# Kernel tuning notes

Measured on AMD Instinct MI355X. Metric: run time of the kernel, lower is better.

The kernel has to match this reference:

```python
import jax, jax.numpy as jnp
import numpy as np

N = 100000
E = 1600000
NEG_SLOPE = 0.2
EPS = 1e-16


def gat_layer(x, src, dst, w, W, a_src, a_dst, b):
    # x: [N, Cin] -> h: [N, Cout]
    h = x @ W
    alpha_src = h @ a_src  # [N]
    alpha_dst = h @ a_dst  # [N]
    # per-edge score: alpha_j + alpha_i, leaky relu, edge-weight adjustment
    alpha = alpha_src[src] + alpha_dst[dst]
    alpha = jax.nn.leaky_relu(alpha, NEG_SLOPE)
    alpha = alpha + (1.0 - 1.0 / w)
    # segment softmax over destination nodes
    m = jax.ops.segment_max(alpha, dst, num_segments=N)
    ea = jnp.exp(alpha - m[dst])
    denom = jax.ops.segment_sum(ea, dst, num_segments=N)
    alpha = ea / (denom[dst] + EPS)
    # scatter-add aggregation of weighted source features
    out = jax.ops.segment_sum(h[src] * alpha[:, None], dst, num_segments=N)
    return out + b


def setup_inputs() -> dict:
    key = jax.random.key(0)
    ks = jax.random.split(key, 12)
    return {
        "x": jax.random.normal(ks[0], (N, 128), dtype=jnp.float32),
        "edge_index": jax.random.randint(ks[1], (2, E), 0, N, dtype=jnp.int64)
        if jax.config.jax_enable_x64 else jax.random.randint(ks[1], (2, E), 0, N, dtype=jnp.int32),
        "edge_weight": jax.random.uniform(ks[2], (E,), dtype=jnp.float32, minval=0.5, maxval=1.5),
        "W1": jax.random.normal(ks[3], (128, 64), dtype=jnp.float32) * 0.08,
        "a_src1": jax.random.normal(ks[4], (64,), dtype=jnp.float32) * 0.1,
        "a_dst1": jax.random.normal(ks[5], (64,), dtype=jnp.float32) * 0.1,
        "b1": jax.random.normal(ks[6], (64,), dtype=jnp.float32) * 0.01,
        "W2": jax.random.normal(ks[7], (64, 7), dtype=jnp.float32) * 0.12,
        "a_src2": jax.random.normal(ks[8], (7,), dtype=jnp.float32) * 0.1,
        "a_dst2": jax.random.normal(ks[9], (7,), dtype=jnp.float32) * 0.1,
        "b2": jax.random.normal(ks[10], (7,), dtype=jnp.float32) * 0.01,
    }


def reference(x, edge_index, edge_weight, W1, a_src1, a_dst1, b1, W2, a_src2, a_dst2, b2):
    # add self loops with edge weight fill_value=1.0 (GATConv default behavior)
    loop = jnp.arange(N, dtype=edge_index.dtype)
    src = jnp.concatenate([edge_index[0], loop])
    dst = jnp.concatenate([edge_index[1], loop])
    w = jnp.concatenate([edge_weight, jnp.ones((N,), dtype=edge_weight.dtype)])
    h = gat_layer(x, src, dst, w, W1, a_src1, a_dst1, b1)
    h = jax.nn.relu(h)  # dropout is identity in eval mode
    out = gat_layer(h, src, dst, w, W2, a_src2, a_dst2, b2)
    return out
```

## Files before the change

### kernel.cpp

```cpp
#include <hip/hip_runtime.h>
#include <hip/hip_bf16.h>

typedef __hip_bfloat16 bf16;

#define DEPS 1e-16f
#define CAP 32
#define OVF_MAX 131072

__device__ __forceinline__ float bfu_lo(unsigned u) { return __uint_as_float(u << 16); }
__device__ __forceinline__ float bfu_hi(unsigned u) { return __uint_as_float(u & 0xffff0000u); }

__device__ __forceinline__ float dec_wt(unsigned u) {
    return (float)(u & 32767u) * (1.f / 8192.f) - 1.1f;
}

__global__ __launch_bounds__(256) void f_gemm_hist(
    const float* __restrict__ x, const float* __restrict__ W1,
    const float* __restrict__ a_src, const float* __restrict__ a_dst,
    bf16* __restrict__ h1, float* __restrict__ asrc, float* __restrict__ adst,
    const int* __restrict__ dstv, int* __restrict__ cnt,
    unsigned char* __restrict__ rank8,
    int N, int E, int T, int gG, int gH)
{
    __shared__ __align__(16) float xl[32 * 128];
    int bid = blockIdx.x;
    int r = bid % 13, chunk = bid / 13;
    int tid = threadIdx.x;

    if (r >= 4) {
        int hb = chunk * 9 + (r - 4);
        if (hb >= gH) return;
        int e = hb * 256 + tid;
        if (e >= T) return;
        int d = (e < E) ? dstv[e] : (e - E);
        int pos = atomicAdd(&cnt[d], 1);
        rank8[e] = (unsigned char)min(pos, 255);
        return;
    }
    int gb = chunk * 4 + r;
    if (gb >= gG) return;
    int n0 = gb * 32;
    for (int i = tid; i < 1024; i += 256) {
        int n = n0 + (i >> 5);
        float4 v = {0.f, 0.f, 0.f, 0.f};
        if (n < N) v = ((const float4*)x)[(size_t)n * 32 + (i & 31)];
        ((float4*)xl)[i] = v;
    }
    __syncthreads();
    int w = tid >> 6, c = tid & 63;
    float sa = a_src[c], da = a_dst[c];
    float acc[8] = {0.f, 0.f, 0.f, 0.f, 0.f, 0.f, 0.f, 0.f};
    const float* Wc = W1 + c;
    for (int k4 = 0; k4 < 32; ++k4) {
        float w0 = Wc[(4 * k4 + 0) * 64];
        float w1 = Wc[(4 * k4 + 1) * 64];
        float w2 = Wc[(4 * k4 + 2) * 64];
        float w3 = Wc[(4 * k4 + 3) * 64];
        #pragma unroll
        for (int i = 0; i < 8; ++i) {
            float4 xv = ((const float4*)(xl + (w * 8 + i) * 128))[k4];
            acc[i] = fmaf(xv.x, w0, fmaf(xv.y, w1,
                     fmaf(xv.z, w2, fmaf(xv.w, w3, acc[i]))));
        }
    }
    #pragma unroll
    for (int i = 0; i < 8; ++i) {
        int n = n0 + w * 8 + i;
        float a = acc[i];
        float ps = a * sa, pd = a * da;
        #pragma unroll
        for (int o = 32; o; o >>= 1) {
            ps += __shfl_xor(ps, o);
            pd += __shfl_xor(pd, o);
        }
        if (n < N) {
            h1[(size_t)n * 64 + c] = __float2bfloat16(a);
            if (c == 0) { asrc[n] = ps; adst[n] = pd; }
        }
    }
}

__global__ __launch_bounds__(256) void f_scatB(
    const int* __restrict__ srcv, const int* __restrict__ dstv,
    const float* __restrict__ ew, const unsigned char* __restrict__ rank8,
    unsigned* __restrict__ bkt, uint2* __restrict__ ovf,
    int* __restrict__ ovfn, int E, int T)
{
    int e = blockIdx.x * 256 + threadIdx.x;
    if (e >= T) return;
    int s, d; float wt;
    if (e < E) { s = srcv[e]; d = dstv[e]; wt = 1.f - 1.f / ew[e]; }
    else       { s = d = e - E; wt = 0.f; }
    unsigned q = (unsigned)((wt + 1.1f) * 8192.f + 0.5f);
    unsigned entry = ((unsigned)s << 15) | q;
    int pos = rank8[e];
    if (pos < CAP) {
        bkt[(size_t)d * CAP + pos] = entry;
    } else {
        int o = atomicAdd(ovfn, 1);
        if (o < OVF_MAX) { uint2 v; v.x = (unsigned)d; v.y = entry; ovf[o] = v; }
    }
}

__global__ __launch_bounds__(256) void f_agg1(
    const int* __restrict__ cnt, const unsigned* __restrict__ bkt,
    const uint2* __restrict__ ovf, const int* __restrict__ ovfn,
    const float* __restrict__ asrc, const float* __restrict__ adst,
    const bf16* __restrict__ h1,
    const float* __restrict__ b1, const float* __restrict__ W2,
    const float* __restrict__ a2s, const float* __restrict__ a2d,
    float* __restrict__ h2p, float* __restrict__ ad2, int N)
{
    __shared__ __align__(16) float WxT[16][68];
    __shared__ __align__(16) float b1l[64];
    __shared__ float2 eb[4][64];
    int tid = threadIdx.x;
    if (tid < 64) {
        float us = 0.f, ud = 0.f;
        #pragma unroll
        for (int c = 0; c < 7; ++c) {
            float wv = W2[tid * 7 + c];
            WxT[c][tid] = wv;
            us = fmaf(wv, a2s[c], us);
            ud = fmaf(wv, a2d[c], ud);
        }
        WxT[7][tid] = us;
        WxT[8][tid] = ud;
        #pragma unroll
        for (int r = 9; r < 16; ++r) WxT[r][tid] = 0.f;
        b1l[tid] = b1[tid];
    }
    __syncthreads();
    int d = blockIdx.x * 4 + (tid >> 6);
    int lane = tid & 63;
    if (d >= N) return;
    int lenf = cnt[d];
    int nc = min(lenf, CAP);
    size_t r0 = (size_t)d * CAP;
    float adv = adst[d];
    int g8 = lane >> 3, l8 = lane & 7;
    float2* ebw = eb[tid >> 6];
    float acc[8] = {0.f, 0.f, 0.f, 0.f, 0.f, 0.f, 0.f, 0.f};
    float sm = 0.f;
    {
        float ea = 0.f; unsigned s = 0;
        if (lane < nc) {
            unsigned u = bkt[r0 + lane];
            s = u >> 15;
            float a = asrc[s] + adv;
            a = (a > 0.f) ? a : 0.2f * a;
            ea = __expf(a + dec_wt(u));
            sm += ea;
        }
        ebw[lane] = make_float2(ea, __uint_as_float(s));
        for (int j = 0; j < nc; j += 8) {
            float2 eq = ebw[j + g8];
            float e = eq.x;
            unsigned sj = __float_as_uint(eq.y);
            uint4 hv = *(const uint4*)&h1[(size_t)sj * 64 + (l8 << 3)];
            acc[0] = fmaf(e, bfu_lo(hv.x), acc[0]);
            acc[1] = fmaf(e, bfu_hi(hv.x), acc[1]);
            acc[2] = fmaf(e, bfu_lo(hv.y), acc[2]);
            acc[3] = fmaf(e, bfu_hi(hv.y), acc[3]);
            acc[4] = fmaf(e, bfu_lo(hv.z), acc[4]);
            acc[5] = fmaf(e, bfu_hi(hv.z), acc[5]);
            acc[6] = fmaf(e, bfu_lo(hv.w), acc[6]);
            acc[7] = fmaf(e, bfu_hi(hv.w), acc[7]);
        }
    }
    if (lenf > CAP) {
        int no = min(*ovfn, OVF_MAX);
        for (int i = g8; i < no; i += 8) {
            uint2 ov = ovf[i];
            if ((int)ov.x == d) {
                unsigned u = ov.y;
                unsigned s = u >> 15;
                float a = asrc[s] + adv;
                a = (a > 0.f) ? a : 0.2f * a;
                float ea = __expf(a + dec_wt(u));
                if (l8 == 0) sm += ea;
                uint4 hv = *(const uint4*)&h1[(size_t)s * 64 + (l8 << 3)];
                acc[0] = fmaf(ea, bfu_lo(hv.x), acc[0]);
                acc[1] = fmaf(ea, bfu_hi(hv.x), acc[1]);
                acc[2] = fmaf(ea, bfu_lo(hv.y), acc[2]);
                acc[3] = fmaf(ea, bfu_hi(hv.y), acc[3]);
                acc[4] = fmaf(ea, bfu_lo(hv.z), acc[4]);
                acc[5] = fmaf(ea, bfu_hi(hv.z), acc[5]);
                acc[6] = fmaf(ea, bfu_lo(hv.w), acc[6]);
                acc[7] = fmaf(ea, bfu_hi(hv.w), acc[7]);
            }
        }
    }
    #pragma unroll
    for (int o = 32; o; o >>= 1) sm += __shfl_xor(sm, o);
    #pragma unroll
    for (int k = 0; k < 8; ++k) {
        acc[k] += __shfl_xor(acc[k], 8);
        acc[k] += __shfl_xor(acc[k], 16);
        acc[k] += __shfl_xor(acc[k], 32);
    }
    float inv = 1.f / (sm + DEPS);
    int c0 = l8 << 3;
    float4 bA = *(const float4*)&b1l[c0];
    float4 bB = *(const float4*)&b1l[c0 + 4];
    float v0 = fmaxf(fmaf(acc[0], inv, bA.x), 0.f);
    float v1 = fmaxf(fmaf(acc[1], inv, bA.y), 0.f);
    float v2 = fmaxf(fmaf(acc[2], inv, bA.z), 0.f);
    float v3 = fmaxf(fmaf(acc[3], inv, bA.w), 0.f);
    float v4 = fmaxf(fmaf(acc[4], inv, bB.x), 0.f);
    float v5 = fmaxf(fmaf(acc[5], inv, bB.y), 0.f);
    float v6 = fmaxf(fmaf(acc[6], inv, bB.z), 0.f);
    float v7 = fmaxf(fmaf(acc[7], inv, bB.w), 0.f);
    float4 wA0 = *(const float4*)&WxT[g8][c0];
    float4 wA1 = *(const float4*)&WxT[g8][c0 + 4];
    float4 wB0 = *(const float4*)&WxT[g8 + 8][c0];
    float4 wB1 = *(const float4*)&WxT[g8 + 8][c0 + 4];
    float rA = fmaf(v0, wA0.x, fmaf(v1, wA0.y, fmaf(v2, wA0.z, fmaf(v3, wA0.w,
               fmaf(v4, wA1.x, fmaf(v5, wA1.y, fmaf(v6, wA1.z, v7 * wA1.w)))))));
    float rB = fmaf(v0, wB0.x, fmaf(v1, wB0.y, fmaf(v2, wB0.z, fmaf(v3, wB0.w,
               fmaf(v4, wB1.x, fmaf(v5, wB1.y, fmaf(v6, wB1.z, v7 * wB1.w)))))));
    rA += __shfl_xor(rA, 1); rA += __shfl_xor(rA, 2); rA += __shfl_xor(rA, 4);
    rB += __shfl_xor(rB, 1); rB += __shfl_xor(rB, 2); rB += __shfl_xor(rB, 4);
    if (l8 == 0) {
        h2p[(size_t)d * 8 + g8] = rA;
        if (g8 == 0) ad2[d] = rB;
    }
}

__global__ __launch_bounds__(256) void f_agg2(
    const int* __restrict__ cnt, const unsigned* __restrict__ bkt,
    const uint2* __restrict__ ovf, const int* __restrict__ ovfn,
    const float* __restrict__ h2p, const float* __restrict__ ad2,
    const float* __restrict__ b2, float* __restrict__ out, int N)
{
    __shared__ float b2l[7];
    if (threadIdx.x < 7) b2l[threadIdx.x] = b2[threadIdx.x];
    __syncthreads();
    int lane = threadIdx.x & 63;
    int wv = threadIdx.x >> 6;
    int grp = lane >> 3, l8 = lane & 7;
    int d = blockIdx.x * 32 + wv * 8 + grp;
    bool valid = d < N;
    int lenf = 0; float adv = 0.f;
    if (valid) { lenf = cnt[d]; adv = ad2[d]; }
    int nc = min(lenf, CAP);
    size_t r0 = (size_t)d * CAP;
    float sm = 0.f;
    float a0 = 0.f, a1 = 0.f, a2 = 0.f, a3 = 0.f, a4 = 0.f, a5 = 0.f, a6 = 0.f;
    for (int p = l8; p < nc; p += 8) {
        unsigned u = bkt[r0 + p];
        int s = (int)(u >> 15);
        const float* hr = &h2p[(size_t)s * 8];
        float4 A = *(const float4*)hr;
        float4 B = *(const float4*)(hr + 4);
        float a = B.w + adv;
        a = (a > 0.f) ? a : 0.2f * a;
        float ea = __expf(a + dec_wt(u));
        sm += ea;
        a0 = fmaf(ea, A.x, a0); a1 = fmaf(ea, A.y, a1);
        a2 = fmaf(ea, A.z, a2); a3 = fmaf(ea, A.w, a3);
        a4 = fmaf(ea, B.x, a4); a5 = fmaf(ea, B.y, a5);
        a6 = fmaf(ea, B.z, a6);
    }
    if (lenf > CAP) {
        int no = min(*ovfn, OVF_MAX);
        for (int i = l8; i < no; i += 8) {
            uint2 ov = ovf[i];
            if ((int)ov.x == d) {
                unsigned u = ov.y;
                int s = (int)(u >> 15);
                const float* hr = &h2p[(size_t)s * 8];
                float4 A = *(const float4*)hr;
                float4 B = *(const float4*)(hr + 4);
                float a = B.w + adv;
                a = (a > 0.f) ? a : 0.2f * a;
                float ea = __expf(a + dec_wt(u));
                sm += ea;
                a0 = fmaf(ea, A.x, a0); a1 = fmaf(ea, A.y, a1);
                a2 = fmaf(ea, A.z, a2); a3 = fmaf(ea, A.w, a3);
                a4 = fmaf(ea, B.x, a4); a5 = fmaf(ea, B.y, a5);
                a6 = fmaf(ea, B.z, a6);
            }
        }
    }
    #pragma unroll
    for (int o = 4; o; o >>= 1) {
        sm += __shfl_xor(sm, o);
        a0 += __shfl_xor(a0, o); a1 += __shfl_xor(a1, o);
        a2 += __shfl_xor(a2, o); a3 += __shfl_xor(a3, o);
        a4 += __shfl_xor(a4, o); a5 += __shfl_xor(a5, o);
        a6 += __shfl_xor(a6, o);
    }
    if (valid && l8 < 7) {
        float inv = 1.f / (sm + DEPS);
        float val = (l8 < 4) ? ((l8 < 2) ? (l8 ? a1 : a0) : ((l8 == 2) ? a2 : a3))
                             : ((l8 < 6) ? ((l8 == 4) ? a4 : a5) : a6);
        out[(size_t)d * 7 + l8] = fmaf(val, inv, b2l[l8]);
    }
}


extern "C" void kernel_launch(void* const* d_in, const int* in_sizes, int n_in,
                              void* d_out, int out_size, void* d_ws, size_t ws_size,
                              hipStream_t stream) {
    const float* x   = (const float*)d_in[0];
    const int*   ei  = (const int*)d_in[1];
    const float* ew  = (const float*)d_in[2];
    const float* W1  = (const float*)d_in[3];
    const float* as1 = (const float*)d_in[4];
    const float* ad1 = (const float*)d_in[5];
    const float* b1  = (const float*)d_in[6];
    const float* W2  = (const float*)d_in[7];
    const float* a2s = (const float*)d_in[8];
    const float* a2d = (const float*)d_in[9];
    const float* b2  = (const float*)d_in[10];

    int N = in_sizes[0] / 128;
    int E = in_sizes[1] / 2;
    int T = E + N;
    const int* srcv = ei;
    const int* dstv = ei + E;
    float* out = (float*)d_out;

    size_t A = 0;
    auto take = [&](size_t b) { size_t o = A; A = (A + b + 255) & ~(size_t)255; return o; };
    size_t o_h1   = take((size_t)N * 64 * 2);
    size_t o_bkt  = take((size_t)N * CAP * 4);
    size_t o_h2p  = take((size_t)N * 8 * 4);
    size_t o_ovf  = take((size_t)OVF_MAX * 8);
    size_t o_cnt  = take((size_t)N * 4);
    size_t o_ovfn = take(256);
    size_t o_asrc = take((size_t)N * 4);
    size_t o_adst = take((size_t)N * 4);
    size_t o_ad2  = take((size_t)N * 4);

    char* base = (char*)d_ws;
    bf16*     h1    = (bf16*)(base + o_h1);
    unsigned* bkt   = (unsigned*)(base + o_bkt);
    float*    h2p   = (float*)(base + o_h2p);
    unsigned char* rank8 = (unsigned char*)(base + o_h2p);
    uint2*    ovf   = (uint2*)(base + o_ovf);
    int*      cnt   = (int*)(base + o_cnt);
    int*      ovfn  = (int*)(base + o_ovfn);
    float*    asrc  = (float*)(base + o_asrc);
    float*    adst  = (float*)(base + o_adst);
    float*    ad2   = (float*)(base + o_ad2);

    int gG = (N + 31) / 32;
    int gH = (T + 255) / 256;
    int chunks = max((gG + 3) / 4, (gH + 8) / 9);
    int gridGH = chunks * 13;
    int gT = (T + 255) / 256;

    hipMemsetAsync(cnt, 0, (size_t)N * 4 + 256, stream);
    f_gemm_hist<<<gridGH, 256, 0, stream>>>(x, W1, as1, ad1, h1, asrc, adst,
                                            dstv, cnt, rank8, N, E, T, gG, gH);
    f_scatB<<<gT, 256, 0, stream>>>(srcv, dstv, ew, rank8, bkt, ovf, ovfn, E, T);
    f_agg1 <<<(N + 3) / 4, 256, 0, stream>>>(cnt, bkt, ovf, ovfn, asrc, adst, h1,
                                             b1, W2, a2s, a2d, h2p, ad2, N);
    f_agg2 <<<(N + 31) / 32, 256, 0, stream>>>(cnt, bkt, ovf, ovfn, h2p, ad2, b2, out, N);
}
```

Measured before the change: 286.5 us.

## Move histogram into its own kernel and fuse bucket scatter with first-layer GEMM

The edge-degree histogram now runs first as a standalone kernel over real edges only. The bucket scatter is then co-scheduled inside the GEMM kernel's spare blocks instead of the histogram. Self-loops are no longer counted by atomics: they take slot cnt[d] directly, and the aggregation kernels add one to the count. The kernel count stays the same, but the scatter now overlaps with the GEMM. In exchange the histogram no longer overlaps with anything, and the self-loop always lands after the real edges, spilling to overflow when the degree is 32 or more.

```diff
diff --git a/kernel.cpp b/kernel.cpp
--- a/kernel.cpp
+++ b/kernel.cpp
@@ -14,13 +14,26 @@
     return (float)(u & 32767u) * (1.f / 8192.f) - 1.1f;
 }
 
-__global__ __launch_bounds__(256) void f_gemm_hist(
+__global__ __launch_bounds__(256) void f_hist(
+    const int* __restrict__ dstv, int* __restrict__ cnt,
+    unsigned char* __restrict__ rank8, int E)
+{
+    int e = blockIdx.x * 256 + threadIdx.x;
+    if (e >= E) return;
+    int d = dstv[e];
+    int pos = atomicAdd(&cnt[d], 1);
+    rank8[e] = (unsigned char)min(pos, 255);
+}
+
+__global__ __launch_bounds__(256) void f_gemm_scat(
     const float* __restrict__ x, const float* __restrict__ W1,
     const float* __restrict__ a_src, const float* __restrict__ a_dst,
     bf16* __restrict__ h1, float* __restrict__ asrc, float* __restrict__ adst,
-    const int* __restrict__ dstv, int* __restrict__ cnt,
-    unsigned char* __restrict__ rank8,
-    int N, int E, int T, int gG, int gH)
+    const int* __restrict__ srcv, const int* __restrict__ dstv,
+    const float* __restrict__ ew, const unsigned char* __restrict__ rank8,
+    const int* __restrict__ cnt,
+    unsigned* __restrict__ bkt, uint2* __restrict__ ovf, int* __restrict__ ovfn,
+    int N, int E, int T, int gG, int gS)
 {
     __shared__ __align__(16) float xl[32 * 128];
     int bid = blockIdx.x;
@@ -28,13 +41,26 @@
     int tid = threadIdx.x;
 
     if (r >= 4) {
-        int hb = chunk * 9 + (r - 4);
-        if (hb >= gH) return;
-        int e = hb * 256 + tid;
+        int sb = chunk * 9 + (r - 4);
+        if (sb >= gS) return;
+        int e = sb * 256 + tid;
         if (e >= T) return;
-        int d = (e < E) ? dstv[e] : (e - E);
-        int pos = atomicAdd(&cnt[d], 1);
-        rank8[e] = (unsigned char)min(pos, 255);
+        int s, d, pos; float wt;
+        if (e < E) {
+            s = srcv[e]; d = dstv[e]; wt = 1.f - 1.f / ew[e];
+            pos = rank8[e];
+        } else {
+            s = d = e - E; wt = 0.f;
+            pos = cnt[d];
+        }
+        unsigned q = (unsigned)((wt + 1.1f) * 8192.f + 0.5f);
+        unsigned entry = ((unsigned)s << 15) | q;
+        if (pos < CAP) {
+            bkt[(size_t)d * CAP + pos] = entry;
+        } else {
+            int o = atomicAdd(ovfn, 1);
+            if (o < OVF_MAX) { uint2 v; v.x = (unsigned)d; v.y = entry; ovf[o] = v; }
+        }
         return;
     }
     int gb = chunk * 4 + r;
@@ -77,28 +103,6 @@
             h1[(size_t)n * 64 + c] = __float2bfloat16(a);
             if (c == 0) { asrc[n] = ps; adst[n] = pd; }
         }
-    }
-}
-
-__global__ __launch_bounds__(256) void f_scatB(
-    const int* __restrict__ srcv, const int* __restrict__ dstv,
-    const float* __restrict__ ew, const unsigned char* __restrict__ rank8,
-    unsigned* __restrict__ bkt, uint2* __restrict__ ovf,
-    int* __restrict__ ovfn, int E, int T)
-{
-    int e = blockIdx.x * 256 + threadIdx.x;
-    if (e >= T) return;
-    int s, d; float wt;
-    if (e < E) { s = srcv[e]; d = dstv[e]; wt = 1.f - 1.f / ew[e]; }
-    else       { s = d = e - E; wt = 0.f; }
-    unsigned q = (unsigned)((wt + 1.1f) * 8192.f + 0.5f);
-    unsigned entry = ((unsigned)s << 15) | q;
-    int pos = rank8[e];
-    if (pos < CAP) {
-        bkt[(size_t)d * CAP + pos] = entry;
-    } else {
-        int o = atomicAdd(ovfn, 1);
-        if (o < OVF_MAX) { uint2 v; v.x = (unsigned)d; v.y = entry; ovf[o] = v; }
     }
 }
 
@@ -134,7 +138,7 @@
     int d = blockIdx.x * 4 + (tid >> 6);
     int lane = tid & 63;
     if (d >= N) return;
-    int lenf = cnt[d];
+    int lenf = cnt[d] + 1;
     int nc = min(lenf, CAP);
     size_t r0 = (size_t)d * CAP;
     float adv = adst[d];
@@ -242,7 +246,7 @@
     int d = blockIdx.x * 32 + wv * 8 + grp;
     bool valid = d < N;
     int lenf = 0; float adv = 0.f;
-    if (valid) { lenf = cnt[d]; adv = ad2[d]; }
+    if (valid) { lenf = cnt[d] + 1; adv = ad2[d]; }
     int nc = min(lenf, CAP);
     size_t r0 = (size_t)d * CAP;
     float sm = 0.f;
@@ -346,16 +350,17 @@
     float*    adst  = (float*)(base + o_adst);
     float*    ad2   = (float*)(base + o_ad2);
 
+    int gE = (E + 255) / 256;
     int gG = (N + 31) / 32;
-    int gH = (T + 255) / 256;
-    int chunks = max((gG + 3) / 4, (gH + 8) / 9);
-    int gridGH = chunks * 13;
-    int gT = (T + 255) / 256;
+    int gS = (T + 255) / 256;
+    int chunks = max((gG + 3) / 4, (gS + 8) / 9);
+    int gridGS = chunks * 13;
 
     hipMemsetAsync(cnt, 0, (size_t)N * 4 + 256, stream);
-    f_gemm_hist<<<gridGH, 256, 0, stream>>>(x, W1, as1, ad1, h1, asrc, adst,
-                                            dstv, cnt, rank8, N, E, T, gG, gH);
-    f_scatB<<<gT, 256, 0, stream>>>(srcv, dstv, ew, rank8, bkt, ovf, ovfn, E, T);
+    f_hist<<<gE, 256, 0, stream>>>(dstv, cnt, rank8, E);
+    f_gemm_scat<<<gridGS, 256, 0, stream>>>(x, W1, as1, ad1, h1, asrc, adst,
+                                            srcv, dstv, ew, rank8, cnt,
+                                            bkt, ovf, ovfn, N, E, T, gG, gS);
     f_agg1 <<<(N + 3) / 4, 256, 0, stream>>>(cnt, bkt, ovf, ovfn, asrc, adst, h1,
                                              b1, W2, a2s, a2d, h2p, ad2, N);
     f_agg2 <<<(N + 31) / 32, 256, 0, stream>>>(cnt, bkt, ovf, ovfn, h2p, ad2, b2, out, N);
```

After: 315.0 us. +9.9%, slower.
